# Kernel tuning notes

Hardware: AMD Instinct MI355X
Metric: run time of the kernel (lower is better)

The kernel has to match this reference:

```python
import jax, jax.numpy as jnp
import numpy as np

N_CHANNELS = 1024
N_HEADS = 16
SEQ = 2048
BATCH = 2


def setup_inputs() -> dict:
    key = jax.random.key(0)
    k1, k2, k3 = jax.random.split(key, 3)
    x = jax.random.normal(k1, (BATCH, SEQ, N_CHANNELS), dtype=jnp.float32)
    qkv_w = jax.random.normal(k2, (3 * N_CHANNELS, N_CHANNELS), dtype=jnp.float32) * 0.02
    qkv_b = jnp.zeros((3 * N_CHANNELS,), dtype=jnp.float32)
    proj_w = jax.random.normal(k3, (N_CHANNELS, N_CHANNELS), dtype=jnp.float32) * 0.02
    proj_b = jnp.zeros((N_CHANNELS,), dtype=jnp.float32)
    return {"x": x, "qkv_w": qkv_w, "qkv_b": qkv_b, "proj_w": proj_w, "proj_b": proj_b}


def reference(x, qkv_w, qkv_b, proj_w, proj_b):
    bs, t, c = x.shape
    h = N_HEADS
    hd = c // h
    scale = hd ** (-0.5)
    # qkv projection: torch Linear is x @ W^T + b
    qkv = x @ qkv_w.T + qkv_b  # [B, T, 3C]
    qkv = qkv.reshape(bs, t, 3, h, hd)
    q, k, v = qkv[:, :, 0], qkv[:, :, 1], qkv[:, :, 2]  # each [B, T, H, hd]
    logits = jnp.einsum('bthc,bshc->bhts', q, k) * scale  # [B, H, T, T]
    # causal mask: log(tril(ones)) -> 0 below diag, -inf above
    causal = jnp.tril(jnp.ones((t, t), dtype=bool))
    logits = jnp.where(causal[None, None], logits, -jnp.inf)
    attn = jax.nn.softmax(logits, axis=-1)
    out = jnp.einsum('bhts,bshc->bthc', attn, v).reshape(bs, t, c)
    out = out @ proj_w.T + proj_b
    return out
```

## Files before the change

### kernel.cpp

```cpp
#include <hip/hip_runtime.h>

typedef __bf16 bf16x8 __attribute__((ext_vector_type(8)));
typedef float f32x4 __attribute__((ext_vector_type(4)));

__device__ inline ushort f2bf(float f) {
    unsigned u = __builtin_bit_cast(unsigned, f);
    unsigned r = (u + 0x7FFFu + ((u >> 16) & 1u)) >> 16;
    return (ushort)r;
}
__device__ inline float bf2f(ushort u) {
    unsigned x = ((unsigned)u) << 16;
    return __builtin_bit_cast(float, x);
}
__device__ inline uint4 pack8(const float* f) {
    uint4 r;
    r.x = (unsigned)f2bf(f[0]) | ((unsigned)f2bf(f[1]) << 16);
    r.y = (unsigned)f2bf(f[2]) | ((unsigned)f2bf(f[3]) << 16);
    r.z = (unsigned)f2bf(f[4]) | ((unsigned)f2bf(f[5]) << 16);
    r.w = (unsigned)f2bf(f[6]) | ((unsigned)f2bf(f[7]) << 16);
    return r;
}

#define MFMA_BF16(a, b, c) __builtin_amdgcn_mfma_f32_16x16x32_bf16(a, b, c, 0, 0, 0)
#define GLDS(g, l) __builtin_amdgcn_global_load_lds( \
    (const __attribute__((address_space(1))) void*)(g), \
    (__attribute__((address_space(3))) void*)(l), 16, 0, 0)

#define QSCALE 0.18033688011112042f

__global__ __launch_bounds__(256) void convert3(
    const float* __restrict__ s0, ushort* __restrict__ d0,
    const float* __restrict__ s1, ushort* __restrict__ d1,
    const float* __restrict__ s2, ushort* __restrict__ d2)
{
    const int i = blockIdx.x * 256 + threadIdx.x;
    const float* s; ushort* d; int off;
    if (i < 524288)      { s = s0; d = d0; off = i; }
    else if (i < 917504) { s = s1; d = d1; off = i - 524288; }
    else                 { s = s2; d = d2; off = i - 917504; }
    const float4* f = (const float4*)s + off * 2;
    float fa[8];
    *(float4*)&fa[0] = f[0];
    *(float4*)&fa[4] = f[1];
    ((uint4*)d)[off] = pack8(fa);
}

__global__ __launch_bounds__(256) void gemm_qkv(
    const ushort* __restrict__ A, const ushort* __restrict__ B,
    const float* __restrict__ bias,
    ushort* __restrict__ outQ, ushort* __restrict__ outK, ushort* __restrict__ outV,
    int N, int K)
{
    __shared__ __align__(16) ushort SMEM[17408];
    ushort* As = SMEM;
    ushort* Bs = SMEM + 8192;

    const int tid = threadIdx.x;
    const int w = tid >> 6;
    const int lane = tid & 63;
    const int l15 = lane & 15;
    const int quad = lane >> 4;
    const int m0 = blockIdx.x * 128;
    const int n0 = blockIdx.y * 128;
    const int wr = (w & 1) * 64;
    const int wc = (w >> 1) * 64;

    f32x4 acc[4][4] = {};

    for (int k0 = 0; k0 < K; k0 += 64) {
        __syncthreads();
#pragma unroll
        for (int j = 0; j < 4; j++) {
            const int r0 = w * 32 + j * 8;
            const int row = r0 + (lane >> 3);
            const int gcol = ((lane & 7) ^ (row & 7)) * 8;
            GLDS(A + (size_t)(m0 + row) * K + k0 + gcol, As + r0 * 64);
            GLDS(B + (size_t)(n0 + row) * K + k0 + gcol, Bs + r0 * 64);
        }
        __syncthreads();

        bf16x8 af[4][2], bf[4][2];
#pragma unroll
        for (int i = 0; i < 4; i++)
#pragma unroll
            for (int kk = 0; kk < 2; kk++) {
                const int ra = wr + i * 16 + l15;
                const int rb = wc + i * 16 + l15;
                af[i][kk] = *(const bf16x8*)&As[ra * 64 + (((kk * 4 + quad) ^ (ra & 7)) * 8)];
                bf[i][kk] = *(const bf16x8*)&Bs[rb * 64 + (((kk * 4 + quad) ^ (rb & 7)) * 8)];
            }
#pragma unroll
        for (int kk = 0; kk < 2; kk++)
#pragma unroll
            for (int mi = 0; mi < 4; mi++)
#pragma unroll
                for (int ni = 0; ni < 4; ni++)
                    acc[mi][ni] = MFMA_BF16(af[mi][kk], bf[ni][kk], acc[mi][ni]);
    }

    const int which = n0 >> 10;
    ushort* Ct = SMEM;
    __syncthreads();
    if (which == 2) {
#pragma unroll
        for (int mi = 0; mi < 4; mi++)
#pragma unroll
            for (int ni = 0; ni < 4; ni++)
#pragma unroll
                for (int r = 0; r < 4; r++) {
                    const int m_loc = wr + mi * 16 + quad * 4 + r;
                    const int n_loc = wc + ni * 16 + l15;
                    Ct[n_loc * 136 + m_loc] =
                        f2bf(acc[mi][ni][r] + bias[n0 + n_loc]);
                }
        __syncthreads();
        const int b = m0 >> 11;
#pragma unroll
        for (int i = 0; i < 8; i++) {
            const int vi = tid + i * 256;
            const int n_loc = vi >> 4, mblk = vi & 15;
            const uint4 val = *(const uint4*)&Ct[n_loc * 136 + mblk * 8];
            const int t = (m0 & 2047) + mblk * 8;
            const int c = (n0 + n_loc) & 1023;
            const int h = c >> 6, d = c & 63;
            *(uint4*)&outV[((size_t)(b * 16 + h) * 64 + d) * 2048 + t] = val;
        }
    } else {
        const float qs = (which == 0) ? QSCALE : 1.0f;
#pragma unroll
        for (int mi = 0; mi < 4; mi++)
#pragma unroll
            for (int ni = 0; ni < 4; ni++)
#pragma unroll
                for (int r = 0; r < 4; r++) {
                    const int m_loc = wr + mi * 16 + quad * 4 + r;
                    const int n_loc = wc + ni * 16 + l15;
                    Ct[m_loc * 136 + n_loc] =
                        f2bf((acc[mi][ni][r] + bias[n0 + n_loc]) * qs);
                }
        __syncthreads();
        ushort* outP = (which == 0) ? outQ : outK;
        const int hb = (n0 & 1023) >> 6;
        const int b = m0 >> 11;
#pragma unroll
        for (int i = 0; i < 8; i++) {
            const int vi = tid + i * 256;
            const int m_loc = vi >> 4, u = vi & 15;
            const uint4 val = *(const uint4*)&Ct[m_loc * 136 + u * 8];
            const int t = (m0 & 2047) + m_loc;
            const int h = hb + (u >> 3);
            const int d8 = (u & 7) * 8;
            *(uint4*)&outP[((size_t)(b * 16 + h)) * 131072 + (size_t)t * 64 + d8] = val;
        }
    }
}

__global__ __launch_bounds__(256) void gemm_proj(
    const ushort* __restrict__ A, const ushort* __restrict__ B,
    const float* __restrict__ bias, float* __restrict__ outD)
{
    const int N = 1024, K = 1024;
    __shared__ __align__(16) ushort SMEM[12288];
    ushort* As = SMEM;
    ushort* Bs = SMEM + 4096;

    const int tid = threadIdx.x;
    const int w = tid >> 6;
    const int lane = tid & 63;
    const int l15 = lane & 15;
    const int quad = lane >> 4;
    const int m0 = blockIdx.x * 64;
    const int n0 = blockIdx.y * 128;
    const int wr = (w & 1) * 32;
    const int wc = (w >> 1) * 64;

    f32x4 acc[2][4] = {};

    for (int k0 = 0; k0 < K; k0 += 64) {
        __syncthreads();
#pragma unroll
        for (int j = 0; j < 2; j++) {
            const int r0 = w * 16 + j * 8;
            const int row = r0 + (lane >> 3);
            const int gcol = ((lane & 7) ^ (row & 7)) * 8;
            GLDS(A + (size_t)(m0 + row) * K + k0 + gcol, As + r0 * 64);
        }
#pragma unroll
        for (int j = 0; j < 4; j++) {
            const int r0 = w * 32 + j * 8;
            const int row = r0 + (lane >> 3);
            const int gcol = ((lane & 7) ^ (row & 7)) * 8;
            GLDS(B + (size_t)(n0 + row) * K + k0 + gcol, Bs + r0 * 64);
        }
        __syncthreads();

        bf16x8 af[2][2], bf[4][2];
#pragma unroll
        for (int kk = 0; kk < 2; kk++) {
#pragma unroll
            for (int mi = 0; mi < 2; mi++) {
                const int ra = wr + mi * 16 + l15;
                af[mi][kk] = *(const bf16x8*)&As[ra * 64 + (((kk * 4 + quad) ^ (ra & 7)) * 8)];
            }
#pragma unroll
            for (int ni = 0; ni < 4; ni++) {
                const int rb = wc + ni * 16 + l15;
                bf[ni][kk] = *(const bf16x8*)&Bs[rb * 64 + (((kk * 4 + quad) ^ (rb & 7)) * 8)];
            }
        }
#pragma unroll
        for (int kk = 0; kk < 2; kk++)
#pragma unroll
            for (int mi = 0; mi < 2; mi++)
#pragma unroll
                for (int ni = 0; ni < 4; ni++)
                    acc[mi][ni] = MFMA_BF16(af[mi][kk], bf[ni][kk], acc[mi][ni]);
    }

    float* Cf = (float*)SMEM;
#pragma unroll
    for (int cch = 0; cch < 2; cch++) {
        __syncthreads();
        if ((wc >> 6) == cch) {
#pragma unroll
            for (int mi = 0; mi < 2; mi++)
#pragma unroll
                for (int ni = 0; ni < 4; ni++)
#pragma unroll
                    for (int r = 0; r < 4; r++) {
                        const int m_loc = wr + mi * 16 + quad * 4 + r;
                        const int nl = ni * 16 + l15;
                        Cf[m_loc * 68 + nl] = acc[mi][ni][r] + bias[n0 + cch * 64 + nl];
                    }
        }
        __syncthreads();
#pragma unroll
        for (int i = 0; i < 4; i++) {
            const int vi = tid + i * 256;
            const int m_loc = vi >> 4, u = vi & 15;
            const float4 val = *(const float4*)&Cf[m_loc * 68 + u * 4];
            *(float4*)&outD[(size_t)(m0 + m_loc) * N + n0 + cch * 64 + u * 4] = val;
        }
    }
}

__global__ __launch_bounds__(256) void attn_split(
    const ushort* __restrict__ Q, const ushort* __restrict__ K,
    const ushort* __restrict__ Vt, ushort* __restrict__ O,
    ushort* __restrict__ Opart, float* __restrict__ Lpart)
{
    __shared__ __align__(16) ushort KV[2][2][64 * 64];
    __shared__ __align__(16) __bf16 Ps[4][16 * 64];

    const int bh = blockIdx.x;
    const int y = blockIdx.y;
    int qt, k0, k1, chunk, split;
    if (y < 48) {
        qt = 31 - (y >> 1); chunk = y & 1; split = 1;
        const int n = qt + 1, h = (n + 1) >> 1;
        k0 = chunk ? h : 0; k1 = chunk ? n : h;
    } else {
        qt = 55 - y; chunk = 0; split = 0; k0 = 0; k1 = qt + 1;
    }
    const int q0 = qt * 64;
    const int tid = threadIdx.x;
    const int w = tid >> 6;
    const int lane = tid & 63;
    const int l15 = lane & 15;
    const int quad = lane >> 4;

    auto stage = [&](int kt, int b) {
        const int t0 = kt * 64;
#pragma unroll
        for (int j = 0; j < 2; j++) {
            const int r0 = w * 16 + j * 8;
            const int row = r0 + (lane >> 3);
            const int gcol = ((lane & 7) ^ (row & 7)) * 8;
            GLDS(K + ((size_t)bh * 2048 + t0 + row) * 64 + gcol, &KV[b][0][r0 * 64]);
            GLDS(Vt + ((size_t)bh * 64 + row) * 2048 + t0 + gcol, &KV[b][1][r0 * 64]);
        }
    };

    const ushort* qbase = Q + ((size_t)bh * 2048 + q0 + w * 16 + l15) * 64;
    bf16x8 qf0 = *(const bf16x8*)(qbase + quad * 8);
    bf16x8 qf1 = *(const bf16x8*)(qbase + 32 + quad * 8);

    bf16x8 ones;
#pragma unroll
    for (int j = 0; j < 8; j++) ones[j] = (__bf16)1.0f;

    f32x4 oacc[4] = {};
    f32x4 lacc = {};

    stage(k0, 0);

    for (int kt = k0; kt < k1; kt++) {
        __syncthreads();
        if (kt + 1 < k1) stage(kt + 1, (kt + 1 - k0) & 1);

        const ushort* Ks = &KV[(kt - k0) & 1][0][0];
        const ushort* Vs = &KV[(kt - k0) & 1][1][0];
        const int t0 = kt * 64;

        f32x4 sacc[4] = {};
#pragma unroll
        for (int cb = 0; cb < 4; cb++) {
            const int rr = cb * 16 + l15;
            bf16x8 b0 = *(const bf16x8*)&Ks[rr * 64 + ((quad ^ (rr & 7)) * 8)];
            bf16x8 b1 = *(const bf16x8*)&Ks[rr * 64 + (((4 + quad) ^ (rr & 7)) * 8)];
            sacc[cb] = MFMA_BF16(qf0, b0, sacc[cb]);
            sacc[cb] = MFMA_BF16(qf1, b1, sacc[cb]);
        }

        __bf16* pw = &Ps[w][0];
        __builtin_amdgcn_wave_barrier();
#pragma unroll
        for (int cb = 0; cb < 4; cb++)
#pragma unroll
            for (int r = 0; r < 4; r++) {
                float x = sacc[cb][r];
                if (kt == qt) {
                    const int col = t0 + cb * 16 + l15;
                    const int row = q0 + w * 16 + quad * 4 + r;
                    if (col > row) x = -1e30f;
                }
                const int prow = quad * 4 + r;
                const int unit = cb * 2 + (l15 >> 3);
                pw[prow * 64 + ((unit ^ (prow & 7)) * 8) + (l15 & 7)] =
                    (__bf16)__builtin_exp2f(x);
            }
        __builtin_amdgcn_s_waitcnt(0xC07F);
        __builtin_amdgcn_wave_barrier();

#pragma unroll
        for (int kc = 0; kc < 2; kc++) {
            bf16x8 afr = *(const bf16x8*)&pw[l15 * 64 + (((kc * 4 + quad) ^ (l15 & 7)) * 8)];
#pragma unroll
            for (int cb = 0; cb < 4; cb++) {
                const int rr = cb * 16 + l15;
                bf16x8 bfr = *(const bf16x8*)&Vs[rr * 64 + (((kc * 4 + quad) ^ (rr & 7)) * 8)];
                oacc[cb] = MFMA_BF16(afr, bfr, oacc[cb]);
            }
            lacc = MFMA_BF16(afr, ones, lacc);
        }
    }

    if (!split) {
        const int b = bh >> 4, h = bh & 15;
#pragma unroll
        for (int r = 0; r < 4; r++) {
            const float inv = 1.0f / lacc[r];
            const int row = q0 + w * 16 + quad * 4 + r;
#pragma unroll
            for (int cb = 0; cb < 4; cb++) {
                const int col = h * 64 + cb * 16 + l15;
                O[((size_t)b * 2048 + row) * 1024 + col] = f2bf(oacc[cb][r] * inv);
            }
        }
    } else {
        const size_t slot2 = ((size_t)bh * 24 + (qt - 8)) * 2 + chunk;
        if (l15 == 0) {
#pragma unroll
            for (int r = 0; r < 4; r++)
                Lpart[slot2 * 64 + w * 16 + quad * 4 + r] = lacc[r];
        }
        __bf16* pw = &Ps[w][0];
        __builtin_amdgcn_wave_barrier();
#pragma unroll
        for (int cb = 0; cb < 4; cb++)
#pragma unroll
            for (int r = 0; r < 4; r++) {
                const int prow = quad * 4 + r;
                const int unit = cb * 2 + (l15 >> 3);
                pw[prow * 64 + ((unit ^ (prow & 7)) * 8) + (l15 & 7)] =
                    (__bf16)oacc[cb][r];
            }
        __builtin_amdgcn_s_waitcnt(0xC07F);
        __builtin_amdgcn_wave_barrier();
        const int r = lane >> 2, u = lane & 3;
        const int p0 = (2 * u) ^ (r & 7), p1 = (2 * u + 1) ^ (r & 7);
        const uint4 a = *(const uint4*)&pw[r * 64 + p0 * 8];
        const uint4 b = *(const uint4*)&pw[r * 64 + p1 * 8];
        ushort* dst = Opart + slot2 * 4096 + (w * 16 + r) * 64 + u * 16;
        *(uint4*)dst = a;
        *(uint4*)(dst + 8) = b;
    }
}

__global__ __launch_bounds__(256) void attn_combine(
    const ushort* __restrict__ Opart, const float* __restrict__ Lpart,
    ushort* __restrict__ O)
{
    const int bh = blockIdx.x;
    const int qt = 8 + blockIdx.y;
    const int tid = threadIdx.x;
    const int row = tid >> 2;
    const int cg = (tid & 3) * 16;
    const size_t s = ((size_t)bh * 24 + (qt - 8)) * 2;
    const ushort* p0 = Opart + s * 4096 + row * 64 + cg;
    const ushort* p1 = p0 + 4096;
    const float inv = 1.0f / (Lpart[s * 64 + row] + Lpart[(s + 1) * 64 + row]);
    const int b = bh >> 4, h = bh & 15;
    ushort* dst = O + ((size_t)b * 2048 + qt * 64 + row) * 1024 + h * 64 + cg;
    ushort out[16];
#pragma unroll
    for (int v = 0; v < 2; v++) {
        uint4 a = *(const uint4*)(p0 + v * 8);
        uint4 c = *(const uint4*)(p1 + v * 8);
        const ushort* ua = (const ushort*)&a;
        const ushort* uc = (const ushort*)&c;
#pragma unroll
        for (int j = 0; j < 8; j++)
            out[v * 8 + j] = f2bf((bf2f(ua[j]) + bf2f(uc[j])) * inv);
    }
    *(uint4*)dst = *(uint4*)&out[0];
    *(uint4*)(dst + 8) = *(uint4*)&out[8];
}

extern "C" void kernel_launch(void* const* d_in, const int* in_sizes, int n_in,
                              void* d_out, int out_size, void* d_ws, size_t ws_size,
                              hipStream_t stream) {
    const float* x      = (const float*)d_in[0];
    const float* qkv_w  = (const float*)d_in[1];
    const float* qkv_b  = (const float*)d_in[2];
    const float* proj_w = (const float*)d_in[3];
    const float* proj_b = (const float*)d_in[4];

    ushort* XbOb  = (ushort*)d_ws + 16;
    ushort* Wqkv  = XbOb + 4194304;
    ushort* Wproj = Wqkv + 3145728;
    ushort* Qb    = Wproj + 1048576;
    ushort* Kb    = Qb + 4194304;
    ushort* Vt    = Kb + 4194304;
    ushort* Opart = Vt + 4194304;
    float*  Lpart = (float*)(Opart + 6291456);

    convert3<<<4096, 256, 0, stream>>>(x, XbOb, qkv_w, Wqkv, proj_w, Wproj);
    gemm_qkv<<<dim3(32, 24), 256, 0, stream>>>(XbOb, Wqkv, qkv_b,
                                               Qb, Kb, Vt, 3072, 1024);
    attn_split<<<dim3(32, 56), 256, 0, stream>>>(Qb, Kb, Vt, XbOb, Opart, Lpart);
    attn_combine<<<dim3(32, 24), 256, 0, stream>>>(Opart, Lpart, XbOb);
    gemm_proj<<<dim3(64, 8), 256, 0, stream>>>(XbOb, Wproj, proj_b, (float*)d_out);
}
```

Baseline: 200.1 us.

## Double-buffer LDS tiles in QKV and projection GEMMs and remap block order

Both GEMM kernels now keep two LDS buffers and issue the global-to-LDS loads for the next K tile before computing on the current one, with a single barrier per iteration. The aim is to overlap memory latency with MFMA work. Block indices are also remapped in a strided, XCD-aware order to improve L2 locality of the A and B panels. The cost is doubled LDS use, which may reduce occupancy, and a dependence on the hardware waiting on outstanding global_load_lds before the barrier.

New measurement: 191.2 us. 4.4% less time.

```diff
diff --git a/kernel.cpp b/kernel.cpp
--- a/kernel.cpp
+++ b/kernel.cpp
@@ -51,34 +51,46 @@
     ushort* __restrict__ outQ, ushort* __restrict__ outK, ushort* __restrict__ outV,
     int N, int K)
 {
-    __shared__ __align__(16) ushort SMEM[17408];
-    ushort* As = SMEM;
-    ushort* Bs = SMEM + 8192;
+    __shared__ __align__(16) ushort SMEM[32768];
 
     const int tid = threadIdx.x;
     const int w = tid >> 6;
     const int lane = tid & 63;
     const int l15 = lane & 15;
     const int quad = lane >> 4;
-    const int m0 = blockIdx.x * 128;
-    const int n0 = blockIdx.y * 128;
+    const int srow = lane >> 3;
+
+    const int bid = blockIdx.x + (blockIdx.y << 5);
+    const int nb = (bid & 7) * 96 + (bid >> 3);
+    const int m0 = (nb / 24) * 128;
+    const int n0 = (nb % 24) * 128;
     const int wr = (w & 1) * 64;
     const int wc = (w >> 1) * 64;
 
-    f32x4 acc[4][4] = {};
-
-    for (int k0 = 0; k0 < K; k0 += 64) {
-        __syncthreads();
+    auto stage = [&](int k0, int buf) {
+        ushort* As = SMEM + buf * 16384;
+        ushort* Bs = As + 8192;
 #pragma unroll
         for (int j = 0; j < 4; j++) {
             const int r0 = w * 32 + j * 8;
-            const int row = r0 + (lane >> 3);
+            const int row = r0 + srow;
             const int gcol = ((lane & 7) ^ (row & 7)) * 8;
             GLDS(A + (size_t)(m0 + row) * K + k0 + gcol, As + r0 * 64);
             GLDS(B + (size_t)(n0 + row) * K + k0 + gcol, Bs + r0 * 64);
         }
-        __syncthreads();
-
+    };
+
+    f32x4 acc[4][4] = {};
+
+    stage(0, 0);
+    __syncthreads();
+
+    for (int k0 = 0; k0 < K; k0 += 64) {
+        const int cur = (k0 >> 6) & 1;
+        if (k0 + 64 < K) stage(k0 + 64, cur ^ 1);
+
+        const ushort* As = SMEM + cur * 16384;
+        const ushort* Bs = As + 8192;
         bf16x8 af[4][2], bf[4][2];
 #pragma unroll
         for (int i = 0; i < 4; i++)
@@ -96,11 +108,11 @@
 #pragma unroll
                 for (int ni = 0; ni < 4; ni++)
                     acc[mi][ni] = MFMA_BF16(af[mi][kk], bf[ni][kk], acc[mi][ni]);
+        __syncthreads();
     }
 
     const int which = n0 >> 10;
     ushort* Ct = SMEM;
-    __syncthreads();
     if (which == 2) {
 #pragma unroll
         for (int mi = 0; mi < 4; mi++)
@@ -160,40 +172,52 @@
     const float* __restrict__ bias, float* __restrict__ outD)
 {
     const int N = 1024, K = 1024;
-    __shared__ __align__(16) ushort SMEM[12288];
-    ushort* As = SMEM;
-    ushort* Bs = SMEM + 4096;
+    __shared__ __align__(16) ushort SMEM[24576];
 
     const int tid = threadIdx.x;
     const int w = tid >> 6;
     const int lane = tid & 63;
     const int l15 = lane & 15;
     const int quad = lane >> 4;
-    const int m0 = blockIdx.x * 64;
-    const int n0 = blockIdx.y * 128;
+    const int srow = lane >> 3;
+
+    const int bid = blockIdx.x + (blockIdx.y << 6);
+    const int nb = (bid & 7) * 64 + (bid >> 3);
+    const int m0 = (nb >> 3) * 64;
+    const int n0 = (nb & 7) * 128;
     const int wr = (w & 1) * 32;
     const int wc = (w >> 1) * 64;
 
-    f32x4 acc[2][4] = {};
-
-    for (int k0 = 0; k0 < K; k0 += 64) {
-        __syncthreads();
+    auto stage = [&](int k0, int buf) {
+        ushort* As = SMEM + buf * 12288;
+        ushort* Bs = As + 4096;
 #pragma unroll
         for (int j = 0; j < 2; j++) {
             const int r0 = w * 16 + j * 8;
-            const int row = r0 + (lane >> 3);
+            const int row = r0 + srow;
             const int gcol = ((lane & 7) ^ (row & 7)) * 8;
             GLDS(A + (size_t)(m0 + row) * K + k0 + gcol, As + r0 * 64);
         }
 #pragma unroll
         for (int j = 0; j < 4; j++) {
             const int r0 = w * 32 + j * 8;
-            const int row = r0 + (lane >> 3);
+            const int row = r0 + srow;
             const int gcol = ((lane & 7) ^ (row & 7)) * 8;
             GLDS(B + (size_t)(n0 + row) * K + k0 + gcol, Bs + r0 * 64);
         }
-        __syncthreads();
-
+    };
+
+    f32x4 acc[2][4] = {};
+
+    stage(0, 0);
+    __syncthreads();
+
+    for (int k0 = 0; k0 < K; k0 += 64) {
+        const int cur = (k0 >> 6) & 1;
+        if (k0 + 64 < K) stage(k0 + 64, cur ^ 1);
+
+        const ushort* As = SMEM + cur * 12288;
+        const ushort* Bs = As + 4096;
         bf16x8 af[2][2], bf[4][2];
 #pragma unroll
         for (int kk = 0; kk < 2; kk++) {
@@ -215,6 +239,7 @@
 #pragma unroll
                 for (int ni = 0; ni < 4; ni++)
                     acc[mi][ni] = MFMA_BF16(af[mi][kk], bf[ni][kk], acc[mi][ni]);
+        __syncthreads();
     }
 
     float* Cf = (float*)SMEM;
```
